# Kernel tuning notes

Measured on AMD Instinct MI355X. Metric: run time of the kernel, lower is better.

Reference implementation:

```python
import jax, jax.numpy as jnp
import numpy as np

D = 768
N_STEPS = 8192


def setup_inputs() -> dict:
    key = jax.random.key(0)
    k1, k2, k3, k4 = jax.random.split(key, 4)
    d = D
    scale = 0.02  # keep the tanh dynamics well-behaved over 8192 Euler steps
    return {
        "x_0": jax.random.normal(k1, (d,), dtype=jnp.float32),
        "tau": jnp.ones((1,), dtype=jnp.float32),
        "Wx": jax.random.normal(k2, (d, d), dtype=jnp.float32) * scale,
        "Wy": jax.random.normal(k3, (d, d), dtype=jnp.float32) * scale,
        "b": jax.random.normal(k4, (d,), dtype=jnp.float32) * scale,
        "N": N_STEPS,
    }


def reference(x_0, tau, Wx, Wy, b, N):
    """Forward-Euler DDE solve of x'(t) = F(x(t), x(t - tau), t) with
    history x(t) = x_0 for t <= 0, dt = tau/10 (N_tau = 10 steps per delay).
    Returns the trajectory as a [d, N+1] array (column k = state at step k),
    matching DDE_adjoint_l.forward / DDE_Solver."""
    N_tau = 10
    dt = tau[0] / N_tau  # dt = 0.1 * tau

    def F(x, y, t):
        # Neural RHS: F(x, x(t - tau), t) = tanh(Wx x + Wy y + b)
        return jnp.tanh(Wx @ x + Wy @ y + b)

    # Ring buffer holding the last N_tau states; x(t)=x_0 for t<=0.
    buf0 = jnp.tile(x_0[None, :], (N_tau, 1))  # [N_tau, d]

    def step(carry, j):
        x, buf = carry
        t = j.astype(jnp.float32) * dt
        y = buf[0]  # x at step j - N_tau (== x_0 while j < N_tau)
        x_next = x + dt * F(x, y, t)
        buf_next = jnp.concatenate([buf[1:], x[None, :]], axis=0)
        return (x_next, buf_next), x

    (x_N, _), xs = jax.lax.scan(step, (x_0, buf0), jnp.arange(N))
    traj = jnp.concatenate([xs, x_N[None, :]], axis=0)  # [N+1, d]
    return traj.T  # [d, N+1]
```

## Files before the change

kernel.cpp:

```cpp
#include <hip/hip_runtime.h>
#include <math.h>


#define DD 768
#define NSTEPS 8192
#define NWG 96
#define NT 256
#define ROWS_PER_WG 8
#define COLS_PER_LANE 24
#define RING 16
#define LSTRIDE 33
#define LSLOT (COLS_PER_LANE * LSTRIDE)

#define RING_OFF 0

typedef __attribute__((ext_vector_type(4))) unsigned int u32x4;
typedef __attribute__((ext_vector_type(2))) unsigned int u32x2;

__device__ __forceinline__ unsigned long long ld_tag(const unsigned long long* p) {
    return __hip_atomic_load(p, __ATOMIC_RELAXED, __HIP_MEMORY_SCOPE_AGENT);
}

__device__ __forceinline__ void sweep_ld(const unsigned long long* p4,
                                         const unsigned long long* p2,
                                         u32x4* q, u32x2* r2) {
    asm volatile("global_load_dwordx4 %0, %2, off sc0 sc1\n\t"
                 "global_load_dwordx2 %1, %3, off sc0 sc1\n\t"
                 "s_waitcnt vmcnt(0)"
                 : "=&v"(*q), "=&v"(*r2)
                 : "v"(p4), "v"(p2)
                 : "memory");
}

__global__ __launch_bounds__(NT, 1)
void ndde_kernel(const float* __restrict__ x0,
                 const float* __restrict__ tau,
                 const float* __restrict__ Wx,
                 const float* __restrict__ Wy,
                 const float* __restrict__ b,
                 float* __restrict__ out,
                 unsigned long long* __restrict__ ring)
{
    __shared__ float hist[RING * LSLOT];

    const int tid = threadIdx.x;
    const int g   = blockIdx.x;
    const int r   = tid >> 5;
    const int c   = tid & 31;
    const int row = g * ROWS_PER_WG + r;
    const int cb  = c * COLS_PER_LANE;

    const float dtf = tau[0] / 10.0f;

    float wxf[COLS_PER_LANE], wyf[COLS_PER_LANE];
    {
        const float* px = Wx + row * DD + cb;
        const float* py = Wy + row * DD + cb;
        #pragma unroll
        for (int i = 0; i < COLS_PER_LANE / 4; ++i) {
            float4 a = *(const float4*)(px + 4 * i);
            wxf[4*i+0] = a.x; wxf[4*i+1] = a.y; wxf[4*i+2] = a.z; wxf[4*i+3] = a.w;
            float4 d2 = *(const float4*)(py + 4 * i);
            wyf[4*i+0] = d2.x; wyf[4*i+1] = d2.y; wyf[4*i+2] = d2.z; wyf[4*i+3] = d2.w;
        }
    }
    #pragma unroll
    for (int i = 0; i < COLS_PER_LANE; ++i) {
        asm volatile("" : "+v"(wxf[i]));
        asm volatile("" : "+v"(wyf[i]));
    }

    const float brow = b[row];
    float xrow = x0[row];
    if (c == 0) out[row * (NSTEPS + 1) + 0] = xrow;

    for (int j = 0; j < NSTEPS; ++j) {
        double dy0 = 0.0, dy1 = 0.0;
        if (j <= 10) {
            const float* ys = x0 + cb;
            #pragma unroll
            for (int i = 0; i < COLS_PER_LANE / 4; ++i) {
                float4 v = *(const float4*)(ys + 4 * i);
                dy0 = fma((double)wyf[4*i+0], (double)v.x, dy0);
                dy1 = fma((double)wyf[4*i+1], (double)v.y, dy1);
                dy0 = fma((double)wyf[4*i+2], (double)v.z, dy0);
                dy1 = fma((double)wyf[4*i+3], (double)v.w, dy1);
            }
        } else {
            const float* hs = hist + ((j - 10) & (RING - 1)) * LSLOT;
            #pragma unroll
            for (int k = 0; k < COLS_PER_LANE; k += 4) {
                float v0 = hs[(k+0)*LSTRIDE + c];
                float v1 = hs[(k+1)*LSTRIDE + c];
                float v2 = hs[(k+2)*LSTRIDE + c];
                float v3 = hs[(k+3)*LSTRIDE + c];
                dy0 = fma((double)wyf[k+0], (double)v0, dy0);
                dy1 = fma((double)wyf[k+1], (double)v1, dy1);
                dy0 = fma((double)wyf[k+2], (double)v2, dy0);
                dy1 = fma((double)wyf[k+3], (double)v3, dy1);
            }
        }
        double doty = dy0 + dy1;
        #pragma unroll
        for (int off = 1; off < 32; off <<= 1)
            doty += __shfl_xor(doty, off);

        if (j >= 1) {
            const unsigned tgt = (unsigned)j;
            const unsigned long long* base = ring + (j & (RING - 1)) * DD;
            const unsigned long long* p4 = base + 2 * tid;
            const unsigned long long* p2 = base + 512 + tid;
            unsigned v0, v1, v2;
            int tries = 0;
            for (;;) {
                bool ok;
                if (tries < 2048) {
                    u32x4 q; u32x2 s;
                    sweep_ld(p4, p2, &q, &s);
                    v0 = q.x; v1 = q.z; v2 = s.x;
                    ok = (q.y == tgt) & (q.w == tgt) & (s.y == tgt);
                } else {
                    unsigned long long q0 = ld_tag(p4 + 0);
                    unsigned long long q1 = ld_tag(p4 + 1);
                    unsigned long long q2 = ld_tag(p2);
                    v0 = (unsigned)q0; v1 = (unsigned)q1; v2 = (unsigned)q2;
                    ok = ((unsigned)(q0 >> 32) == tgt) &
                         ((unsigned)(q1 >> 32) == tgt) &
                         ((unsigned)(q2 >> 32) == tgt);
                }
                if (__all(ok)) break;
                ++tries;
            }
            float* hsw = hist + (j & (RING - 1)) * LSLOT;
            const int iA = 2 * tid, iB = 2 * tid + 1, iC = 512 + tid;
            hsw[(iA % 24) * LSTRIDE + (iA / 24)] = __uint_as_float(v0);
            hsw[(iB % 24) * LSTRIDE + (iB / 24)] = __uint_as_float(v1);
            hsw[(iC % 24) * LSTRIDE + (iC / 24)] = __uint_as_float(v2);
            __syncthreads();
        }

        double dx0 = 0.0, dx1 = 0.0;
        if (j == 0) {
            const float* xs = x0 + cb;
            #pragma unroll
            for (int i = 0; i < COLS_PER_LANE / 4; ++i) {
                float4 v = *(const float4*)(xs + 4 * i);
                dx0 = fma((double)wxf[4*i+0], (double)v.x, dx0);
                dx1 = fma((double)wxf[4*i+1], (double)v.y, dx1);
                dx0 = fma((double)wxf[4*i+2], (double)v.z, dx0);
                dx1 = fma((double)wxf[4*i+3], (double)v.w, dx1);
            }
        } else {
            const float* hs = hist + (j & (RING - 1)) * LSLOT;
            #pragma unroll
            for (int k = 0; k < COLS_PER_LANE; k += 4) {
                float v0 = hs[(k+0)*LSTRIDE + c];
                float v1 = hs[(k+1)*LSTRIDE + c];
                float v2 = hs[(k+2)*LSTRIDE + c];
                float v3 = hs[(k+3)*LSTRIDE + c];
                dx0 = fma((double)wxf[k+0], (double)v0, dx0);
                dx1 = fma((double)wxf[k+1], (double)v1, dx1);
                dx0 = fma((double)wxf[k+2], (double)v2, dx0);
                dx1 = fma((double)wxf[k+3], (double)v3, dx1);
            }
        }
        double dotx = dx0 + dx1;
        #pragma unroll
        for (int off = 1; off < 32; off <<= 1)
            dotx += __shfl_xor(dotx, off);

        if (c == 0) {
            float z = __fadd_rn(__fadd_rn((float)dotx, (float)doty), brow);
            float th;
            float az = fabsf(z);
            if (az < 9.3f) th = (float)tanh((double)z);
            else           th = (z > 0.0f) ? 1.0f : -1.0f;
            xrow = __fadd_rn(xrow, __fmul_rn(dtf, th));

            unsigned long long pack =
                ((unsigned long long)(unsigned)(j + 1) << 32) |
                (unsigned long long)__float_as_uint(xrow);
            __hip_atomic_store(&ring[((j + 1) & (RING - 1)) * DD + row], pack,
                               __ATOMIC_RELAXED, __HIP_MEMORY_SCOPE_AGENT);

            out[row * (NSTEPS + 1) + (j + 1)] = xrow;
        }
    }
}

extern "C" void kernel_launch(void* const* d_in, const int* in_sizes, int n_in,
                              void* d_out, int out_size, void* d_ws, size_t ws_size,
                              hipStream_t stream) {
    (void)in_sizes; (void)n_in; (void)out_size; (void)ws_size;

    const float* x0  = (const float*)d_in[0];
    const float* tau = (const float*)d_in[1];
    const float* Wx  = (const float*)d_in[2];
    const float* Wy  = (const float*)d_in[3];
    const float* b   = (const float*)d_in[4];
    float* out = (float*)d_out;

    unsigned long long* ring = (unsigned long long*)((char*)d_ws + RING_OFF);

    ndde_kernel<<<NWG, NT, 0, stream>>>(x0, tau, Wx, Wy, b, out, ring);
}
```

Before: 14.25 ms.

## Use 64 workgroups of 384 threads and issue speculative ring load early

Cuts the grid from 96 workgroups of 256 threads to 64 of 384, each owning 12 rows. With 384 threads, each thread polls exactly two packed ring entries with a single dwordx4 load, so the second dwordx2 load goes away. The first poll is now issued as a speculative volatile load at the top of the step, so its latency overlaps the Wy dot product, and the spin loop only runs if that early read is stale. The cost is fewer workgroups taking part in the grid-wide handoff and more rows per workgroup, and the speculative read may often be stale and need re-polling.

Result: slower. 21.52 ms (+51.1%).

```diff
diff --git a/kernel.cpp b/kernel.cpp
--- a/kernel.cpp
+++ b/kernel.cpp
@@ -4,9 +4,9 @@
 
 #define DD 768
 #define NSTEPS 8192
-#define NWG 96
-#define NT 256
-#define ROWS_PER_WG 8
+#define NWG 64
+#define NT 384
+#define ROWS_PER_WG 12
 #define COLS_PER_LANE 24
 #define RING 16
 #define LSTRIDE 33
@@ -15,21 +15,17 @@
 #define RING_OFF 0
 
 typedef __attribute__((ext_vector_type(4))) unsigned int u32x4;
-typedef __attribute__((ext_vector_type(2))) unsigned int u32x2;
 
 __device__ __forceinline__ unsigned long long ld_tag(const unsigned long long* p) {
     return __hip_atomic_load(p, __ATOMIC_RELAXED, __HIP_MEMORY_SCOPE_AGENT);
 }
 
-__device__ __forceinline__ void sweep_ld(const unsigned long long* p4,
-                                         const unsigned long long* p2,
-                                         u32x4* q, u32x2* r2) {
-    asm volatile("global_load_dwordx4 %0, %2, off sc0 sc1\n\t"
-                 "global_load_dwordx2 %1, %3, off sc0 sc1\n\t"
+__device__ __forceinline__ u32x4 ld_pair(const unsigned long long* p) {
+    u32x4 v;
+    asm volatile("global_load_dwordx4 %0, %1, off sc0 sc1\n\t"
                  "s_waitcnt vmcnt(0)"
-                 : "=&v"(*q), "=&v"(*r2)
-                 : "v"(p4), "v"(p2)
-                 : "memory");
+                 : "=v"(v) : "v"(p) : "memory");
+    return v;
 }
 
 __global__ __launch_bounds__(NT, 1)
@@ -75,6 +71,14 @@
     if (c == 0) out[row * (NSTEPS + 1) + 0] = xrow;
 
     for (int j = 0; j < NSTEPS; ++j) {
+        const unsigned long long* base = ring + (j & (RING - 1)) * DD;
+        const unsigned long long* p4   = base + 2 * tid;
+
+        u32x4 spec;
+        if (j >= 1) {
+            spec = *(const volatile u32x4*)p4;
+        }
+
         double dy0 = 0.0, dy1 = 0.0;
         if (j <= 10) {
             const float* ys = x0 + cb;
@@ -107,35 +111,34 @@
 
         if (j >= 1) {
             const unsigned tgt = (unsigned)j;
-            const unsigned long long* base = ring + (j & (RING - 1)) * DD;
-            const unsigned long long* p4 = base + 2 * tid;
-            const unsigned long long* p2 = base + 512 + tid;
-            unsigned v0, v1, v2;
+            unsigned v0, v1;
+            bool got;
+            {
+                bool ok = (spec.y == tgt) & (spec.w == tgt);
+                got = __all(ok);
+                v0 = spec.x; v1 = spec.z;
+            }
             int tries = 0;
-            for (;;) {
+            while (!got) {
                 bool ok;
                 if (tries < 2048) {
-                    u32x4 q; u32x2 s;
-                    sweep_ld(p4, p2, &q, &s);
-                    v0 = q.x; v1 = q.z; v2 = s.x;
-                    ok = (q.y == tgt) & (q.w == tgt) & (s.y == tgt);
+                    u32x4 q = ld_pair(p4);
+                    v0 = q.x; v1 = q.z;
+                    ok = (q.y == tgt) & (q.w == tgt);
                 } else {
                     unsigned long long q0 = ld_tag(p4 + 0);
                     unsigned long long q1 = ld_tag(p4 + 1);
-                    unsigned long long q2 = ld_tag(p2);
-                    v0 = (unsigned)q0; v1 = (unsigned)q1; v2 = (unsigned)q2;
+                    v0 = (unsigned)q0; v1 = (unsigned)q1;
                     ok = ((unsigned)(q0 >> 32) == tgt) &
-                         ((unsigned)(q1 >> 32) == tgt) &
-                         ((unsigned)(q2 >> 32) == tgt);
+                         ((unsigned)(q1 >> 32) == tgt);
                 }
-                if (__all(ok)) break;
+                got = __all(ok);
                 ++tries;
             }
             float* hsw = hist + (j & (RING - 1)) * LSLOT;
-            const int iA = 2 * tid, iB = 2 * tid + 1, iC = 512 + tid;
+            const int iA = 2 * tid, iB = 2 * tid + 1;
             hsw[(iA % 24) * LSTRIDE + (iA / 24)] = __uint_as_float(v0);
             hsw[(iB % 24) * LSTRIDE + (iB / 24)] = __uint_as_float(v1);
-            hsw[(iC % 24) * LSTRIDE + (iC / 24)] = __uint_as_float(v2);
             __syncthreads();
         }
 
```
